# Kernel tuning notes

Measured on AMD Instinct MI355X. Metric: run time of the kernel, lower is better.

## Reference

```python
import jax, jax.numpy as jnp
import numpy as np

B, C, H, W = 2, 64, 64, 128
HW = H * W
PCR = (0.0, -25.6, -3.0, 51.2, 25.6, 1.0)  # point cloud range x/y/z min, x/y/z max
VOX = (0.1, 0.1, 4.0)                      # voxel size
NX = int(round((PCR[3] - PCR[0]) / VOX[0]))  # 512
NY = int(round((PCR[4] - PCR[1]) / VOX[1]))  # 512
BIG = 1e10  # masked-out distance (avoid inf for clean vjp)


def _rand_points(key):
    k_xyz, k_i = jax.random.split(key)
    u = jax.random.uniform(k_xyz, (B, 3, H, W), jnp.float32)
    lo = jnp.array([PCR[0], PCR[1], PCR[2]], jnp.float32).reshape(1, 3, 1, 1)
    hi = jnp.array([PCR[3], PCR[4], PCR[5]], jnp.float32).reshape(1, 3, 1, 1)
    xyz = lo + u * (hi - lo)
    inten = jax.random.uniform(k_i, (B, 1, H, W), jnp.float32)
    return jnp.concatenate([xyz, inten], axis=1)  # (B,4,H,W)


def setup_inputs() -> dict:
    key = jax.random.key(0)
    k1, k2, k3, k4, k5 = jax.random.split(key, 5)
    return {
        "fv_features": jax.random.normal(k1, (B, C, H, W), jnp.float32),
        "points_img": _rand_points(k2),
        "proj_masks": jax.random.randint(k4, (B, H, W), 0, 2).astype(jnp.int32),
        "points_img_far": _rand_points(k3),
        "proj_masks_far": jax.random.randint(k5, (B, H, W), 0, 2).astype(jnp.int32),
    }


def _three_interpolate(near_pts, near_feats, near_valid, far_pts):
    """pointnet2 three_nn + three_interpolate with invalid near points masked.
    near_pts: (N,3), near_feats: (N,C), near_valid: (N,) bool, far_pts: (M,3).
    Returns interpolated far features (M,C)."""
    # squared distances via |a|^2 + |b|^2 - 2 a.b  -> (M, N), avoids (M,N,3) temp
    d2 = (jnp.sum(far_pts * far_pts, -1)[:, None]
          + jnp.sum(near_pts * near_pts, -1)[None, :]
          - 2.0 * far_pts @ near_pts.T)
    d2 = jnp.where(near_valid[None, :], d2, BIG)
    neg_d, idx = jax.lax.top_k(-d2, 3)        # 3 nearest near-points per far point
    dist = -neg_d                              # squared dists, as in pointnet2 CUDA
    dist_recip = 1.0 / (dist + 1e-8)
    weight = dist_recip / jnp.sum(dist_recip, axis=-1, keepdims=True)  # (M,3)
    gathered = near_feats[idx]                 # (M,3,C)
    return jnp.einsum('mk,mkc->mc', weight, gathered)


def _scatter_bev(pts, feats, valid):
    """Mean-scatter point features into the BEV grid. pts:(N,3) feats:(N,C) valid:(N,)."""
    ix = jnp.floor((pts[:, 0] - PCR[0]) / VOX[0]).astype(jnp.int32)
    iy = jnp.floor((pts[:, 1] - PCR[1]) / VOX[1]).astype(jnp.int32)
    in_range = (ix >= 0) & (ix < NX) & (iy >= 0) & (iy < NY)
    w = (valid & in_range).astype(feats.dtype)            # zero-weight invalid pts
    flat = jnp.clip(iy, 0, NY - 1) * NX + jnp.clip(ix, 0, NX - 1)
    sums = jnp.zeros((NY * NX, feats.shape[1]), feats.dtype).at[flat].add(feats * w[:, None])
    cnt = jnp.zeros((NY * NX,), feats.dtype).at[flat].add(w)
    bev = sums / jnp.maximum(cnt, 1.0)[:, None]
    return bev.reshape(NY, NX, -1).transpose(2, 0, 1)      # (C, NY, NX)


def reference(fv_features, points_img, proj_masks, points_img_far, proj_masks_far):
    feats = fv_features.transpose(0, 2, 3, 1).reshape(B, HW, C)
    pts = points_img[:, :3].transpose(0, 2, 3, 1).reshape(B, HW, 3)
    pts_far = points_img_far[:, :3].transpose(0, 2, 3, 1).reshape(B, HW, 3)
    m = proj_masks.reshape(B, HW) > 0
    m_far = proj_masks_far.reshape(B, HW) > 0
    outs = []
    for k in range(B):  # small fixed batch loop, mirrors original per-sample loop
        interp = _three_interpolate(pts[k], feats[k], m[k], pts_far[k])
        all_pts = jnp.concatenate([pts[k], pts_far[k]], axis=0)
        all_feats = jnp.concatenate([feats[k], interp], axis=0)
        all_valid = jnp.concatenate([m[k], m_far[k]], axis=0)
        outs.append(_scatter_bev(all_pts, all_feats, all_valid))
    return jnp.stack(outs, axis=0)  # (B, C, NY, NX)
```

## Files before the change

kernel.cpp:

```cpp
#include <hip/hip_runtime.h>
#include <math.h>

constexpr int B_  = 2;
constexpr int C_  = 64;
constexpr int HW_ = 64 * 128;
constexpr int N_  = HW_;
constexpr int NX_ = 512;
constexpr int NY_ = 512;
constexpr int NYNX_ = NX_ * NY_;
constexpr int GC_  = 32;
constexpr int GCC_ = GC_ * GC_;
constexpr int CAP_ = 48;
constexpr int LPF_ = 8;
constexpr int BN_  = B_ * N_;
constexpr int NNB_ = BN_ / 32;
constexpr int NSB_ = BN_ / 32;

__device__ __forceinline__ int voxel_of(float x, float y, float w) {
#pragma clang fp contract(off)
  if (w == 0.0f) return -1;
  float qx = (x - 0.0f) / 0.1f;
  float qy = (y - (-25.6f)) / 0.1f;
  int ix = (int)floorf(qx);
  int iy = (int)floorf(qy);
  if (ix < 0 || ix >= NX_ || iy < 0 || iy >= NY_) return -1;
  return iy * NX_ + ix;
}

__device__ __forceinline__ int gcell_x(float x) {
  int c = (int)floorf(x * 0.625f);
  return min(GC_ - 1, max(0, c));
}
__device__ __forceinline__ int gcell_y(float y) {
  int c = (int)floorf((y + 25.6f) * 0.625f);
  return min(GC_ - 1, max(0, c));
}

__device__ __forceinline__ int wave_append(int* ctr) {
  unsigned long long mk = __ballot(1);
  int lane = threadIdx.x & 63;
  int lead = __ffsll((unsigned long long)mk) - 1;
  int basep = 0;
  if (lane == lead) basep = atomicAdd(ctr, __popcll(mk));
  basep = __shfl(basep, lead);
  return basep + __popcll(mk & ((1ull << lane) - 1ull));
}

__global__ __launch_bounds__(256) void prep_kernel(
    const float* __restrict__ fv,
    const float* __restrict__ pi, const int* __restrict__ pm,
    const float* __restrict__ pif, const int* __restrict__ pmf,
    float* __restrict__ cnt, int* __restrict__ gcellcnt,
    int* __restrict__ nctr, float4* __restrict__ farlist,
    int2* __restrict__ nearlist,
    float4* __restrict__ gpts, int* __restrict__ gidx,
    float* __restrict__ acc, float* __restrict__ fvT) {
#pragma clang fp contract(off)
  __shared__ float tile[64][65];
  if (blockIdx.x < 64) {
    int t = blockIdx.x * 256 + threadIdx.x;
    int k = t / N_, n = t % N_;
    const float* base  = pi  + (size_t)k * 4 * HW_;
    const float* basef = pif + (size_t)k * 4 * HW_;
    float x = base[n], y = base[HW_ + n], z = base[2 * HW_ + n];
    bool v = pm[k * HW_ + n] > 0;
    float fx = basef[n], fy = basef[HW_ + n], fz = basef[2 * HW_ + n];
    bool vf = pmf[k * HW_ + n] > 0;

    if (v) {
      float sq = (x * x + y * y) + z * z;
      int c = gcell_y(y) * GC_ + gcell_x(x);
      int p = atomicAdd(&gcellcnt[k * GCC_ + c], 1);
      if (p < CAP_) {
        size_t o = (size_t)(k * GCC_ + c) * CAP_ + p;
        gpts[o] = make_float4(x, y, z, sq);
        gidx[o] = n;
      }
    }

    float4 z4 = make_float4(0.0f, 0.0f, 0.0f, 0.0f);
    int vn = voxel_of(x, y, v ? 1.0f : 0.0f);
    if (vn >= 0) {
      int kv = k * NYNX_ + vn;
      float old = atomicAdd(&cnt[kv], 1.0f);
      if (old == 1.0f) {
        float4* row = (float4*)(acc + (size_t)kv * C_);
#pragma unroll
        for (int i = 0; i < C_ / 4; ++i) row[i] = z4;
      }
      int p = wave_append(&nctr[1]);
      nearlist[p] = make_int2(kv, t);
    }
    int vfv = voxel_of(fx, fy, vf ? 1.0f : 0.0f);
    if (vfv >= 0) {
      int kv = k * NYNX_ + vfv;
      float old2 = atomicAdd(&cnt[kv], 1.0f);
      if (old2 == 1.0f) {
        float4* row = (float4*)(acc + (size_t)kv * C_);
#pragma unroll
        for (int i = 0; i < C_ / 4; ++i) row[i] = z4;
      }
      int p = wave_append(&nctr[0]);
      farlist[p] = make_float4(fx, fy, fz, __int_as_float(kv));
    }
  } else {
    int bid = blockIdx.x - 64;
    int k = bid >> 7;
    int n0 = (bid & 127) * 64;
    int tx = threadIdx.x & 63, ty = threadIdx.x >> 6;
    for (int c = ty; c < C_; c += 4)
      tile[c][tx] = fv[((size_t)(k * C_ + c)) * HW_ + n0 + tx];
    __syncthreads();
    for (int nn = ty; nn < 64; nn += 4)
      fvT[((size_t)(k * HW_ + n0 + nn)) * C_ + tx] = tile[tx][nn];
  }
}

__device__ __forceinline__ void merge3L(float tv, int idx,
                                        float& b0, float& b1, float& b2,
                                        int& i0, int& i1, int& i2) {
  bool w0 = (tv < b0) || (tv == b0 && idx < i0);
  bool w1 = (tv < b1) || (tv == b1 && idx < i1);
  bool w2 = (tv < b2) || (tv == b2 && idx < i2);
  float ob0 = b0, ob1 = b1;
  int   oi0 = i0, oi1 = i1;
  b0 = w0 ? tv : b0;                    i0 = w0 ? idx : i0;
  b1 = w0 ? ob0 : (w1 ? tv : b1);       i1 = w0 ? oi0 : (w1 ? idx : i1);
  b2 = w1 ? ob1 : (w2 ? tv : b2);       i2 = w1 ? oi1 : (w2 ? idx : i2);
}

__global__ __launch_bounds__(256) void nn_scatter_kernel(
    const int* __restrict__ nctr,
    const float4* __restrict__ farlist, const int2* __restrict__ nearlist,
    const int* __restrict__ gcellcnt,
    const float4* __restrict__ gpts, const int* __restrict__ gidx,
    const float* __restrict__ fvT,
    const float* __restrict__ cnt, float* __restrict__ acc) {
#pragma clang fp contract(off)
  int tid = threadIdx.x;
  if (blockIdx.x < (unsigned)NNB_) {
    int q = tid & (LPF_ - 1);
    int g = blockIdx.x * (256 / LPF_) + (tid / LPF_);
    if (g >= nctr[0]) return;

    float4 f = farlist[g];
    int kv = __float_as_int(f.w);
    int k = kv >> 18;

    float sf = (f.x * f.x + f.y * f.y) + f.z * f.z;
    float ax = 2.0f * f.x, ay = 2.0f * f.y, az = 2.0f * f.z;
    int fcx = gcell_x(f.x), fcy = gcell_y(f.y);
    const int* gcc_ = gcellcnt + k * GCC_;

    float b0 = 1e30f, b1 = 1e30f, b2 = 1e30f;
    int i0 = 0, i1 = 0, i2 = 0;

    for (int r = 0; r < GC_; ++r) {
      int nc = (r == 0) ? 1 : 8 * r;
      for (int i = q; i < nc; i += LPF_) {
        int dx, dy;
        if (r == 0)            { dx = 0;             dy = 0; }
        else if (i < 2*r + 1)  { dx = i - r;         dy = -r; }
        else if (i < 4*r + 2)  { dx = i - (3*r + 1); dy = r; }
        else if (i < 6*r + 1)  { dx = -r;            dy = i - (5*r + 1); }
        else                   { dx = r;             dy = i - 7*r; }
        int cx = fcx + dx, cy = fcy + dy;
        if (cx < 0 || cx >= GC_ || cy < 0 || cy >= GC_) continue;
        int c = cy * GC_ + cx;
        int e = gcc_[c];
        if (e > CAP_) e = CAP_;
        const float4* gp = gpts + (size_t)(k * GCC_ + c) * CAP_;
        const int*    gi = gidx + (size_t)(k * GCC_ + c) * CAP_;
        for (int j = 0; j < e; ++j) {
          float4 p = gp[j];
          int idx = gi[j];
          float p0 = ax * p.x;
          float mm = __builtin_fmaf(az, p.z, __builtin_fmaf(ay, p.y, p0));
          float tv = (sf + p.w) - mm;
          merge3L(tv, idx, b0, b1, b2, i0, i1, i2);
        }
      }
      float s2 = b2;
      s2 = fminf(s2, __shfl_xor(s2, 1));
      s2 = fminf(s2, __shfl_xor(s2, 2));
      s2 = fminf(s2, __shfl_xor(s2, 4));
      float rd = (float)r * 1.6f;
      if (rd * rd > s2 + 0.01f) break;
    }

    int base = tid & ~(LPF_ - 1);
    for (int s = 1; s < LPF_; ++s) {
      float v0 = __shfl(b0, base + s), v1 = __shfl(b1, base + s), v2 = __shfl(b2, base + s);
      int   j0 = __shfl(i0, base + s), j1 = __shfl(i1, base + s), j2 = __shfl(i2, base + s);
      if (q == 0) {
        merge3L(v0, j0, b0, b1, b2, i0, i1, i2);
        merge3L(v1, j1, b0, b1, b2, i0, i1, i2);
        merge3L(v2, j2, b0, b1, b2, i0, i1, i2);
      }
    }
    float w0_ = 0.0f, w1_ = 0.0f, w2_ = 0.0f;
    if (q == 0) {
      float r0 = 1.0f / (b0 + 1e-8f);
      float r1 = 1.0f / (b1 + 1e-8f);
      float r2 = 1.0f / (b2 + 1e-8f);
      float rs = (r0 + r1) + r2;
      w0_ = r0 / rs; w1_ = r1 / rs; w2_ = r2 / rs;
    }
    float w0 = __shfl(w0_, base), w1 = __shfl(w1_, base), w2 = __shfl(w2_, base);
    int   j0 = __shfl(i0, base),  j1 = __shfl(i1, base),  j2 = __shfl(i2, base);

    float cn = cnt[kv];
    size_t rowoff = (size_t)kv * C_;
    const float4* r0p = (const float4*)(fvT + ((size_t)(k * N_ + j0)) * C_);
    const float4* r1p = (const float4*)(fvT + ((size_t)(k * N_ + j1)) * C_);
    const float4* r2p = (const float4*)(fvT + ((size_t)(k * N_ + j2)) * C_);
#pragma unroll
    for (int h = 0; h < 2; ++h) {
      int c4 = q * 2 + h;
      float4 a = r0p[c4], b = r1p[c4], c = r2p[c4];
      float4 val;
      val.x = (w0 * a.x + w1 * b.x) + w2 * c.x;
      val.y = (w0 * a.y + w1 * b.y) + w2 * c.y;
      val.z = (w0 * a.z + w1 * b.z) + w2 * c.z;
      val.w = (w0 * a.w + w1 * b.w) + w2 * c.w;
      if (cn == 1.0f) {
        ((float4*)(acc + rowoff))[c4] = val;
      } else {
        float* p = acc + rowoff + c4 * 4;
        atomicAdd(p + 0, val.x); atomicAdd(p + 1, val.y);
        atomicAdd(p + 2, val.z); atomicAdd(p + 3, val.w);
      }
    }
  } else {
    int q = tid & 7;
    int g = (blockIdx.x - NNB_) * 32 + (tid >> 3);
    if (g >= nctr[1]) return;
    int2 e = nearlist[g];
    int kv = e.x;
    float cn = cnt[kv];
    size_t rowoff = (size_t)kv * C_;
    const float4* src = (const float4*)(fvT + (size_t)e.y * C_);
#pragma unroll
    for (int h = 0; h < 2; ++h) {
      int c4 = q * 2 + h;
      float4 val = src[c4];
      if (cn == 1.0f) {
        ((float4*)(acc + rowoff))[c4] = val;
      } else {
        float* p = acc + rowoff + c4 * 4;
        atomicAdd(p + 0, val.x); atomicAdd(p + 1, val.y);
        atomicAdd(p + 2, val.z); atomicAdd(p + 3, val.w);
      }
    }
  }
}

__global__ __launch_bounds__(256) void emit_kernel(
    const float* __restrict__ acc, const float* __restrict__ cnt,
    float* __restrict__ out) {
#pragma clang fp contract(off)
  __shared__ float tile[64][65];
  __shared__ float cs[64];
  int t = threadIdx.x;
  int k = blockIdx.y;
  int v0 = blockIdx.x * 64;

  if (t < 64) cs[t] = cnt[(size_t)k * NYNX_ + v0 + t];
  __syncthreads();

  const float4* acc4 = (const float4*)acc;
#pragma unroll
  for (int p = 0; p < 4; ++p) {
    int row = p * 16 + (t >> 4);
    int f4  = t & 15;
    float c = cs[row];
    float4 a = make_float4(0.0f, 0.0f, 0.0f, 0.0f);
    if (c > 0.0f) {
      a = acc4[((size_t)k * NYNX_ + v0 + row) * (C_ / 4) + f4];
      a.x /= c; a.y /= c; a.z /= c; a.w /= c;
    }
    tile[f4 * 4 + 0][row] = a.x;
    tile[f4 * 4 + 1][row] = a.y;
    tile[f4 * 4 + 2][row] = a.z;
    tile[f4 * 4 + 3][row] = a.w;
  }
  __syncthreads();

#pragma unroll
  for (int p = 0; p < 4; ++p) {
    int c  = p * 16 + (t >> 4);
    int xq = t & 15;
    float4 o = make_float4(tile[c][xq * 4 + 0], tile[c][xq * 4 + 1],
                           tile[c][xq * 4 + 2], tile[c][xq * 4 + 3]);
    ((float4*)out)[(((size_t)k * C_ + c) * NYNX_ + v0) / 4 + xq] = o;
  }
}

extern "C" void kernel_launch(void* const* d_in, const int* in_sizes, int n_in,
                              void* d_out, int out_size, void* d_ws, size_t ws_size,
                              hipStream_t stream) {
  const float* fv  = (const float*)d_in[0];
  const float* pi  = (const float*)d_in[1];
  const int*   pm  = (const int*)d_in[2];
  const float* pif = (const float*)d_in[3];
  const int*   pmf = (const int*)d_in[4];
  float* out = (float*)d_out;

  char* wsb = (char*)d_ws;
  float*  fvT     = (float*)(wsb);
  float*  cnt     = (float*)(wsb + 4194304);
  int*    gcell   = (int*)(wsb + 6291456);
  int*    nctr    = (int*)(wsb + 6299648);
  float4* farlist = (float4*)(wsb + 6299664);
  int2*   nearlist= (int2*)(wsb + 6561808);
  float4* gpts    = (float4*)(wsb + 6692880);
  int*    gidx    = (int*)(wsb + 8265744);
  float*  acc     = (float*)(wsb + 16777216);

  hipMemsetAsync(cnt, 0, 2105360, stream);

  prep_kernel<<<320, 256, 0, stream>>>(
      fv, pi, pm, pif, pmf, cnt, gcell, nctr, farlist, nearlist,
      gpts, gidx, acc, fvT);
  nn_scatter_kernel<<<NNB_ + NSB_, 256, 0, stream>>>(
      nctr, farlist, nearlist, gcell, gpts, gidx, fvT, cnt, acc);
  emit_kernel<<<dim3(NYNX_ / 64, B_), 256, 0, stream>>>(acc, cnt, out);
}
```

Measured before the change: 182.8 us.

## Fuse memset, prep, NN-scatter and emit into one cooperative kernel with grid syncs

Replaces the memset and three kernel launches with a single cooperative kernel of 1024 blocks. Grid-wide syncs separate four phases: zeroing counters, prep, NN/scatter and emit. The emit phase loops eight tiles per block to cover the grid. The aim is to remove launch gaps and the separate memset. In exchange it adds grid-sync cost, a launch-bound occupancy constraint and less parallel slack in the emit phase.

```diff
diff --git a/kernel.cpp b/kernel.cpp
--- a/kernel.cpp
+++ b/kernel.cpp
@@ -1,5 +1,8 @@
 #include <hip/hip_runtime.h>
+#include <hip/hip_cooperative_groups.h>
 #include <math.h>
+
+namespace cg = cooperative_groups;
 
 constexpr int B_  = 2;
 constexpr int C_  = 64;
@@ -14,7 +17,8 @@
 constexpr int LPF_ = 8;
 constexpr int BN_  = B_ * N_;
 constexpr int NNB_ = BN_ / 32;
-constexpr int NSB_ = BN_ / 32;
+constexpr int GRID_ = 1024;
+constexpr int ZERO4_ = 131585;
 
 __device__ __forceinline__ int voxel_of(float x, float y, float w) {
 #pragma clang fp contract(off)
@@ -44,76 +48,6 @@
   if (lane == lead) basep = atomicAdd(ctr, __popcll(mk));
   basep = __shfl(basep, lead);
   return basep + __popcll(mk & ((1ull << lane) - 1ull));
-}
-
-__global__ __launch_bounds__(256) void prep_kernel(
-    const float* __restrict__ fv,
-    const float* __restrict__ pi, const int* __restrict__ pm,
-    const float* __restrict__ pif, const int* __restrict__ pmf,
-    float* __restrict__ cnt, int* __restrict__ gcellcnt,
-    int* __restrict__ nctr, float4* __restrict__ farlist,
-    int2* __restrict__ nearlist,
-    float4* __restrict__ gpts, int* __restrict__ gidx,
-    float* __restrict__ acc, float* __restrict__ fvT) {
-#pragma clang fp contract(off)
-  __shared__ float tile[64][65];
-  if (blockIdx.x < 64) {
-    int t = blockIdx.x * 256 + threadIdx.x;
-    int k = t / N_, n = t % N_;
-    const float* base  = pi  + (size_t)k * 4 * HW_;
-    const float* basef = pif + (size_t)k * 4 * HW_;
-    float x = base[n], y = base[HW_ + n], z = base[2 * HW_ + n];
-    bool v = pm[k * HW_ + n] > 0;
-    float fx = basef[n], fy = basef[HW_ + n], fz = basef[2 * HW_ + n];
-    bool vf = pmf[k * HW_ + n] > 0;
-
-    if (v) {
-      float sq = (x * x + y * y) + z * z;
-      int c = gcell_y(y) * GC_ + gcell_x(x);
-      int p = atomicAdd(&gcellcnt[k * GCC_ + c], 1);
-      if (p < CAP_) {
-        size_t o = (size_t)(k * GCC_ + c) * CAP_ + p;
-        gpts[o] = make_float4(x, y, z, sq);
-        gidx[o] = n;
-      }
-    }
-
-    float4 z4 = make_float4(0.0f, 0.0f, 0.0f, 0.0f);
-    int vn = voxel_of(x, y, v ? 1.0f : 0.0f);
-    if (vn >= 0) {
-      int kv = k * NYNX_ + vn;
-      float old = atomicAdd(&cnt[kv], 1.0f);
-      if (old == 1.0f) {
-        float4* row = (float4*)(acc + (size_t)kv * C_);
-#pragma unroll
-        for (int i = 0; i < C_ / 4; ++i) row[i] = z4;
-      }
-      int p = wave_append(&nctr[1]);
-      nearlist[p] = make_int2(kv, t);
-    }
-    int vfv = voxel_of(fx, fy, vf ? 1.0f : 0.0f);
-    if (vfv >= 0) {
-      int kv = k * NYNX_ + vfv;
-      float old2 = atomicAdd(&cnt[kv], 1.0f);
-      if (old2 == 1.0f) {
-        float4* row = (float4*)(acc + (size_t)kv * C_);
-#pragma unroll
-        for (int i = 0; i < C_ / 4; ++i) row[i] = z4;
-      }
-      int p = wave_append(&nctr[0]);
-      farlist[p] = make_float4(fx, fy, fz, __int_as_float(kv));
-    }
-  } else {
-    int bid = blockIdx.x - 64;
-    int k = bid >> 7;
-    int n0 = (bid & 127) * 64;
-    int tx = threadIdx.x & 63, ty = threadIdx.x >> 6;
-    for (int c = ty; c < C_; c += 4)
-      tile[c][tx] = fv[((size_t)(k * C_ + c)) * HW_ + n0 + tx];
-    __syncthreads();
-    for (int nn = ty; nn < 64; nn += 4)
-      fvT[((size_t)(k * HW_ + n0 + nn)) * C_ + tx] = tile[tx][nn];
-  }
 }
 
 __device__ __forceinline__ void merge3L(float tv, int idx,
@@ -129,170 +63,241 @@
   b2 = w1 ? ob1 : (w2 ? tv : b2);       i2 = w1 ? oi1 : (w2 ? idx : i2);
 }
 
-__global__ __launch_bounds__(256) void nn_scatter_kernel(
-    const int* __restrict__ nctr,
-    const float4* __restrict__ farlist, const int2* __restrict__ nearlist,
-    const int* __restrict__ gcellcnt,
-    const float4* __restrict__ gpts, const int* __restrict__ gidx,
-    const float* __restrict__ fvT,
-    const float* __restrict__ cnt, float* __restrict__ acc) {
+__global__ __launch_bounds__(256, 4) void fused_kernel(
+    const float* __restrict__ fv,
+    const float* __restrict__ pi, const int* __restrict__ pm,
+    const float* __restrict__ pif, const int* __restrict__ pmf,
+    float* __restrict__ cnt, int* __restrict__ gcellcnt,
+    int* __restrict__ nctr, float4* __restrict__ farlist,
+    int2* __restrict__ nearlist, float4* __restrict__ gpts,
+    int* __restrict__ gidx, float* __restrict__ fvT,
+    float* __restrict__ acc, float* __restrict__ out) {
 #pragma clang fp contract(off)
+  cg::grid_group grid = cg::this_grid();
+  __shared__ float tile[64][65];
+  __shared__ float cs[64];
   int tid = threadIdx.x;
-  if (blockIdx.x < (unsigned)NNB_) {
+  int bid = blockIdx.x;
+
+  {
+    int idx = bid * 256 + tid;
+    if (idx < ZERO4_)
+      ((float4*)cnt)[idx] = make_float4(0.0f, 0.0f, 0.0f, 0.0f);
+  }
+  grid.sync();
+
+  if (bid < 64) {
+    int t = bid * 256 + tid;
+    int k = t / N_, n = t % N_;
+    const float* base  = pi  + (size_t)k * 4 * HW_;
+    const float* basef = pif + (size_t)k * 4 * HW_;
+    float x = base[n], y = base[HW_ + n], z = base[2 * HW_ + n];
+    bool v = pm[k * HW_ + n] > 0;
+    float fx = basef[n], fy = basef[HW_ + n], fz = basef[2 * HW_ + n];
+    bool vf = pmf[k * HW_ + n] > 0;
+
+    if (v) {
+      float sq = (x * x + y * y) + z * z;
+      int c = gcell_y(y) * GC_ + gcell_x(x);
+      int p = atomicAdd(&gcellcnt[k * GCC_ + c], 1);
+      if (p < CAP_) {
+        size_t o = (size_t)(k * GCC_ + c) * CAP_ + p;
+        gpts[o] = make_float4(x, y, z, sq);
+        gidx[o] = n;
+      }
+    }
+
+    float4 z4 = make_float4(0.0f, 0.0f, 0.0f, 0.0f);
+    int vn = voxel_of(x, y, v ? 1.0f : 0.0f);
+    if (vn >= 0) {
+      int kv = k * NYNX_ + vn;
+      float old = atomicAdd(&cnt[kv], 1.0f);
+      if (old == 1.0f) {
+        float4* row = (float4*)(acc + (size_t)kv * C_);
+#pragma unroll
+        for (int i = 0; i < C_ / 4; ++i) row[i] = z4;
+      }
+      int p = wave_append(&nctr[1]);
+      nearlist[p] = make_int2(kv, t);
+    }
+    int vfv = voxel_of(fx, fy, vf ? 1.0f : 0.0f);
+    if (vfv >= 0) {
+      int kv = k * NYNX_ + vfv;
+      float old2 = atomicAdd(&cnt[kv], 1.0f);
+      if (old2 == 1.0f) {
+        float4* row = (float4*)(acc + (size_t)kv * C_);
+#pragma unroll
+        for (int i = 0; i < C_ / 4; ++i) row[i] = z4;
+      }
+      int p = wave_append(&nctr[0]);
+      farlist[p] = make_float4(fx, fy, fz, __int_as_float(kv));
+    }
+  } else if (bid < 320) {
+    int bt = bid - 64;
+    int k = bt >> 7;
+    int n0 = (bt & 127) * 64;
+    int tx = tid & 63, ty = tid >> 6;
+    for (int c = ty; c < C_; c += 4)
+      tile[c][tx] = fv[((size_t)(k * C_ + c)) * HW_ + n0 + tx];
+    __syncthreads();
+    for (int nn = ty; nn < 64; nn += 4)
+      fvT[((size_t)(k * HW_ + n0 + nn)) * C_ + tx] = tile[tx][nn];
+  }
+  grid.sync();
+
+  if (bid < NNB_) {
     int q = tid & (LPF_ - 1);
-    int g = blockIdx.x * (256 / LPF_) + (tid / LPF_);
-    if (g >= nctr[0]) return;
-
-    float4 f = farlist[g];
-    int kv = __float_as_int(f.w);
-    int k = kv >> 18;
-
-    float sf = (f.x * f.x + f.y * f.y) + f.z * f.z;
-    float ax = 2.0f * f.x, ay = 2.0f * f.y, az = 2.0f * f.z;
-    int fcx = gcell_x(f.x), fcy = gcell_y(f.y);
-    const int* gcc_ = gcellcnt + k * GCC_;
-
-    float b0 = 1e30f, b1 = 1e30f, b2 = 1e30f;
-    int i0 = 0, i1 = 0, i2 = 0;
-
-    for (int r = 0; r < GC_; ++r) {
-      int nc = (r == 0) ? 1 : 8 * r;
-      for (int i = q; i < nc; i += LPF_) {
-        int dx, dy;
-        if (r == 0)            { dx = 0;             dy = 0; }
-        else if (i < 2*r + 1)  { dx = i - r;         dy = -r; }
-        else if (i < 4*r + 2)  { dx = i - (3*r + 1); dy = r; }
-        else if (i < 6*r + 1)  { dx = -r;            dy = i - (5*r + 1); }
-        else                   { dx = r;             dy = i - 7*r; }
-        int cx = fcx + dx, cy = fcy + dy;
-        if (cx < 0 || cx >= GC_ || cy < 0 || cy >= GC_) continue;
-        int c = cy * GC_ + cx;
-        int e = gcc_[c];
-        if (e > CAP_) e = CAP_;
-        const float4* gp = gpts + (size_t)(k * GCC_ + c) * CAP_;
-        const int*    gi = gidx + (size_t)(k * GCC_ + c) * CAP_;
-        for (int j = 0; j < e; ++j) {
-          float4 p = gp[j];
-          int idx = gi[j];
-          float p0 = ax * p.x;
-          float mm = __builtin_fmaf(az, p.z, __builtin_fmaf(ay, p.y, p0));
-          float tv = (sf + p.w) - mm;
-          merge3L(tv, idx, b0, b1, b2, i0, i1, i2);
+    int g = bid * (256 / LPF_) + (tid / LPF_);
+    if (g < nctr[0]) {
+      float4 f = farlist[g];
+      int kv = __float_as_int(f.w);
+      int k = kv >> 18;
+
+      float sf = (f.x * f.x + f.y * f.y) + f.z * f.z;
+      float ax = 2.0f * f.x, ay = 2.0f * f.y, az = 2.0f * f.z;
+      int fcx = gcell_x(f.x), fcy = gcell_y(f.y);
+      const int* gcc_ = gcellcnt + k * GCC_;
+
+      float b0 = 1e30f, b1 = 1e30f, b2 = 1e30f;
+      int i0 = 0, i1 = 0, i2 = 0;
+
+      for (int r = 0; r < GC_; ++r) {
+        int nc = (r == 0) ? 1 : 8 * r;
+        for (int i = q; i < nc; i += LPF_) {
+          int dx, dy;
+          if (r == 0)            { dx = 0;             dy = 0; }
+          else if (i < 2*r + 1)  { dx = i - r;         dy = -r; }
+          else if (i < 4*r + 2)  { dx = i - (3*r + 1); dy = r; }
+          else if (i < 6*r + 1)  { dx = -r;            dy = i - (5*r + 1); }
+          else                   { dx = r;             dy = i - 7*r; }
+          int cx = fcx + dx, cy = fcy + dy;
+          if (cx < 0 || cx >= GC_ || cy < 0 || cy >= GC_) continue;
+          int c = cy * GC_ + cx;
+          int e = gcc_[c];
+          if (e > CAP_) e = CAP_;
+          const float4* gp = gpts + (size_t)(k * GCC_ + c) * CAP_;
+          const int*    gi = gidx + (size_t)(k * GCC_ + c) * CAP_;
+          for (int j = 0; j < e; ++j) {
+            float4 p = gp[j];
+            int idx = gi[j];
+            float p0 = ax * p.x;
+            float mm = __builtin_fmaf(az, p.z, __builtin_fmaf(ay, p.y, p0));
+            float tv = (sf + p.w) - mm;
+            merge3L(tv, idx, b0, b1, b2, i0, i1, i2);
+          }
         }
-      }
-      float s2 = b2;
-      s2 = fminf(s2, __shfl_xor(s2, 1));
-      s2 = fminf(s2, __shfl_xor(s2, 2));
-      s2 = fminf(s2, __shfl_xor(s2, 4));
-      float rd = (float)r * 1.6f;
-      if (rd * rd > s2 + 0.01f) break;
-    }
-
-    int base = tid & ~(LPF_ - 1);
-    for (int s = 1; s < LPF_; ++s) {
-      float v0 = __shfl(b0, base + s), v1 = __shfl(b1, base + s), v2 = __shfl(b2, base + s);
-      int   j0 = __shfl(i0, base + s), j1 = __shfl(i1, base + s), j2 = __shfl(i2, base + s);
+        float s2 = b2;
+        s2 = fminf(s2, __shfl_xor(s2, 1));
+        s2 = fminf(s2, __shfl_xor(s2, 2));
+        s2 = fminf(s2, __shfl_xor(s2, 4));
+        float rd = (float)r * 1.6f;
+        if (rd * rd > s2 + 0.01f) break;
+      }
+
+      int base = tid & ~(LPF_ - 1);
+      for (int s = 1; s < LPF_; ++s) {
+        float v0 = __shfl(b0, base + s), v1 = __shfl(b1, base + s), v2 = __shfl(b2, base + s);
+        int   j0 = __shfl(i0, base + s), j1 = __shfl(i1, base + s), j2 = __shfl(i2, base + s);
+        if (q == 0) {
+          merge3L(v0, j0, b0, b1, b2, i0, i1, i2);
+          merge3L(v1, j1, b0, b1, b2, i0, i1, i2);
+          merge3L(v2, j2, b0, b1, b2, i0, i1, i2);
+        }
+      }
+      float w0_ = 0.0f, w1_ = 0.0f, w2_ = 0.0f;
       if (q == 0) {
-        merge3L(v0, j0, b0, b1, b2, i0, i1, i2);
-        merge3L(v1, j1, b0, b1, b2, i0, i1, i2);
-        merge3L(v2, j2, b0, b1, b2, i0, i1, i2);
-      }
-    }
-    float w0_ = 0.0f, w1_ = 0.0f, w2_ = 0.0f;
-    if (q == 0) {
-      float r0 = 1.0f / (b0 + 1e-8f);
-      float r1 = 1.0f / (b1 + 1e-8f);
-      float r2 = 1.0f / (b2 + 1e-8f);
-      float rs = (r0 + r1) + r2;
-      w0_ = r0 / rs; w1_ = r1 / rs; w2_ = r2 / rs;
-    }
-    float w0 = __shfl(w0_, base), w1 = __shfl(w1_, base), w2 = __shfl(w2_, base);
-    int   j0 = __shfl(i0, base),  j1 = __shfl(i1, base),  j2 = __shfl(i2, base);
-
-    float cn = cnt[kv];
-    size_t rowoff = (size_t)kv * C_;
-    const float4* r0p = (const float4*)(fvT + ((size_t)(k * N_ + j0)) * C_);
-    const float4* r1p = (const float4*)(fvT + ((size_t)(k * N_ + j1)) * C_);
-    const float4* r2p = (const float4*)(fvT + ((size_t)(k * N_ + j2)) * C_);
-#pragma unroll
-    for (int h = 0; h < 2; ++h) {
-      int c4 = q * 2 + h;
-      float4 a = r0p[c4], b = r1p[c4], c = r2p[c4];
-      float4 val;
-      val.x = (w0 * a.x + w1 * b.x) + w2 * c.x;
-      val.y = (w0 * a.y + w1 * b.y) + w2 * c.y;
-      val.z = (w0 * a.z + w1 * b.z) + w2 * c.z;
-      val.w = (w0 * a.w + w1 * b.w) + w2 * c.w;
-      if (cn == 1.0f) {
-        ((float4*)(acc + rowoff))[c4] = val;
-      } else {
-        float* p = acc + rowoff + c4 * 4;
-        atomicAdd(p + 0, val.x); atomicAdd(p + 1, val.y);
-        atomicAdd(p + 2, val.z); atomicAdd(p + 3, val.w);
+        float r0 = 1.0f / (b0 + 1e-8f);
+        float r1 = 1.0f / (b1 + 1e-8f);
+        float r2 = 1.0f / (b2 + 1e-8f);
+        float rs = (r0 + r1) + r2;
+        w0_ = r0 / rs; w1_ = r1 / rs; w2_ = r2 / rs;
+      }
+      float w0 = __shfl(w0_, base), w1 = __shfl(w1_, base), w2 = __shfl(w2_, base);
+      int   j0 = __shfl(i0, base),  j1 = __shfl(i1, base),  j2 = __shfl(i2, base);
+
+      float cn = cnt[kv];
+      size_t rowoff = (size_t)kv * C_;
+      const float4* r0p = (const float4*)(fvT + ((size_t)(k * N_ + j0)) * C_);
+      const float4* r1p = (const float4*)(fvT + ((size_t)(k * N_ + j1)) * C_);
+      const float4* r2p = (const float4*)(fvT + ((size_t)(k * N_ + j2)) * C_);
+#pragma unroll
+      for (int h = 0; h < 2; ++h) {
+        int c4 = q * 2 + h;
+        float4 a = r0p[c4], b = r1p[c4], c = r2p[c4];
+        float4 val;
+        val.x = (w0 * a.x + w1 * b.x) + w2 * c.x;
+        val.y = (w0 * a.y + w1 * b.y) + w2 * c.y;
+        val.z = (w0 * a.z + w1 * b.z) + w2 * c.z;
+        val.w = (w0 * a.w + w1 * b.w) + w2 * c.w;
+        if (cn == 1.0f) {
+          ((float4*)(acc + rowoff))[c4] = val;
+        } else {
+          float* p = acc + rowoff + c4 * 4;
+          atomicAdd(p + 0, val.x); atomicAdd(p + 1, val.y);
+          atomicAdd(p + 2, val.z); atomicAdd(p + 3, val.w);
+        }
       }
     }
   } else {
     int q = tid & 7;
-    int g = (blockIdx.x - NNB_) * 32 + (tid >> 3);
-    if (g >= nctr[1]) return;
-    int2 e = nearlist[g];
-    int kv = e.x;
-    float cn = cnt[kv];
-    size_t rowoff = (size_t)kv * C_;
-    const float4* src = (const float4*)(fvT + (size_t)e.y * C_);
-#pragma unroll
-    for (int h = 0; h < 2; ++h) {
-      int c4 = q * 2 + h;
-      float4 val = src[c4];
-      if (cn == 1.0f) {
-        ((float4*)(acc + rowoff))[c4] = val;
-      } else {
-        float* p = acc + rowoff + c4 * 4;
-        atomicAdd(p + 0, val.x); atomicAdd(p + 1, val.y);
-        atomicAdd(p + 2, val.z); atomicAdd(p + 3, val.w);
+    int g = (bid - NNB_) * 32 + (tid >> 3);
+    if (g < nctr[1]) {
+      int2 e = nearlist[g];
+      int kv = e.x;
+      float cn = cnt[kv];
+      size_t rowoff = (size_t)kv * C_;
+      const float4* src = (const float4*)(fvT + (size_t)e.y * C_);
+#pragma unroll
+      for (int h = 0; h < 2; ++h) {
+        int c4 = q * 2 + h;
+        float4 val = src[c4];
+        if (cn == 1.0f) {
+          ((float4*)(acc + rowoff))[c4] = val;
+        } else {
+          float* p = acc + rowoff + c4 * 4;
+          atomicAdd(p + 0, val.x); atomicAdd(p + 1, val.y);
+          atomicAdd(p + 2, val.z); atomicAdd(p + 3, val.w);
+        }
       }
     }
   }
-}
-
-__global__ __launch_bounds__(256) void emit_kernel(
-    const float* __restrict__ acc, const float* __restrict__ cnt,
-    float* __restrict__ out) {
-#pragma clang fp contract(off)
-  __shared__ float tile[64][65];
-  __shared__ float cs[64];
-  int t = threadIdx.x;
-  int k = blockIdx.y;
-  int v0 = blockIdx.x * 64;
-
-  if (t < 64) cs[t] = cnt[(size_t)k * NYNX_ + v0 + t];
-  __syncthreads();
+  grid.sync();
 
   const float4* acc4 = (const float4*)acc;
-#pragma unroll
-  for (int p = 0; p < 4; ++p) {
-    int row = p * 16 + (t >> 4);
-    int f4  = t & 15;
-    float c = cs[row];
-    float4 a = make_float4(0.0f, 0.0f, 0.0f, 0.0f);
-    if (c > 0.0f) {
-      a = acc4[((size_t)k * NYNX_ + v0 + row) * (C_ / 4) + f4];
-      a.x /= c; a.y /= c; a.z /= c; a.w /= c;
-    }
-    tile[f4 * 4 + 0][row] = a.x;
-    tile[f4 * 4 + 1][row] = a.y;
-    tile[f4 * 4 + 2][row] = a.z;
-    tile[f4 * 4 + 3][row] = a.w;
-  }
-  __syncthreads();
-
-#pragma unroll
-  for (int p = 0; p < 4; ++p) {
-    int c  = p * 16 + (t >> 4);
-    int xq = t & 15;
-    float4 o = make_float4(tile[c][xq * 4 + 0], tile[c][xq * 4 + 1],
-                           tile[c][xq * 4 + 2], tile[c][xq * 4 + 3]);
-    ((float4*)out)[(((size_t)k * C_ + c) * NYNX_ + v0) / 4 + xq] = o;
+  for (int it = 0; it < 8; ++it) {
+    int tt = bid * 8 + it;
+    int k  = tt >> 12;
+    int v0 = (tt & 4095) * 64;
+
+    if (tid < 64) cs[tid] = cnt[(size_t)k * NYNX_ + v0 + tid];
+    __syncthreads();
+
+#pragma unroll
+    for (int p = 0; p < 4; ++p) {
+      int row = p * 16 + (tid >> 4);
+      int f4  = tid & 15;
+      float c = cs[row];
+      float4 a = make_float4(0.0f, 0.0f, 0.0f, 0.0f);
+      if (c > 0.0f) {
+        a = acc4[((size_t)k * NYNX_ + v0 + row) * (C_ / 4) + f4];
+        a.x /= c; a.y /= c; a.z /= c; a.w /= c;
+      }
+      tile[f4 * 4 + 0][row] = a.x;
+      tile[f4 * 4 + 1][row] = a.y;
+      tile[f4 * 4 + 2][row] = a.z;
+      tile[f4 * 4 + 3][row] = a.w;
+    }
+    __syncthreads();
+
+#pragma unroll
+    for (int p = 0; p < 4; ++p) {
+      int c  = p * 16 + (tid >> 4);
+      int xq = tid & 15;
+      float4 o = make_float4(tile[c][xq * 4 + 0], tile[c][xq * 4 + 1],
+                             tile[c][xq * 4 + 2], tile[c][xq * 4 + 3]);
+      ((float4*)out)[(((size_t)k * C_ + c) * NYNX_ + v0) / 4 + xq] = o;
+    }
+    __syncthreads();
   }
 }
 
@@ -317,12 +322,10 @@
   int*    gidx    = (int*)(wsb + 8265744);
   float*  acc     = (float*)(wsb + 16777216);
 
-  hipMemsetAsync(cnt, 0, 2105360, stream);
-
-  prep_kernel<<<320, 256, 0, stream>>>(
-      fv, pi, pm, pif, pmf, cnt, gcell, nctr, farlist, nearlist,
-      gpts, gidx, acc, fvT);
-  nn_scatter_kernel<<<NNB_ + NSB_, 256, 0, stream>>>(
-      nctr, farlist, nearlist, gcell, gpts, gidx, fvT, cnt, acc);
-  emit_kernel<<<dim3(NYNX_ / 64, B_), 256, 0, stream>>>(acc, cnt, out);
-}
+  void* args[] = {(void*)&fv, (void*)&pi, (void*)&pm, (void*)&pif, (void*)&pmf,
+                  (void*)&cnt, (void*)&gcell, (void*)&nctr, (void*)&farlist,
+                  (void*)&nearlist, (void*)&gpts, (void*)&gidx, (void*)&fvT,
+                  (void*)&acc, (void*)&out};
+  hipLaunchCooperativeKernel((const void*)fused_kernel, dim3(GRID_), dim3(256),
+                             args, 0, stream);
+}
```

Result: slower. 449.9 us (+146.1%).
